# Kernel tuning notes

Measured on AMD Instinct MI355X. Metric: run time of the kernel, lower is better.

The kernel has to match this reference:

```python
import jax, jax.numpy as jnp
import numpy as np

V, E, H = 50257, 256, 256   # vocab/output_size, embed_size, hidden_size
T, B = 4096, 64             # encoder time steps, batch


def setup_inputs() -> dict:
    key = jax.random.key(0)
    ks = jax.random.split(key, 12)
    s = 0.05
    return {
        "input_ids": jax.random.randint(ks[0], (B,), 0, V),
        "hidden": jax.random.normal(ks[1], (1, B, H), dtype=jnp.float32) * s,
        "encoder_outputs": jax.random.normal(ks[2], (T, B, 2 * H), dtype=jnp.float32) * s,
        # learned parameters (PyTorch Linear convention: W @ x.T, W shape (out, in))
        "emb": jax.random.normal(ks[3], (V, E), dtype=jnp.float32) * s,
        "W_attn": jax.random.normal(ks[4], (H, 3 * H), dtype=jnp.float32) * s,
        "b_attn": jnp.zeros((H,), jnp.float32),
        "v": jax.random.normal(ks[5], (H,), dtype=jnp.float32) * s,
        "W_comb": jax.random.normal(ks[6], (H, 2 * H + E), dtype=jnp.float32) * s,
        "b_comb": jnp.zeros((H,), jnp.float32),
        "W_ih": jax.random.normal(ks[7], (3 * H, H), dtype=jnp.float32) * s,
        "W_hh": jax.random.normal(ks[8], (3 * H, H), dtype=jnp.float32) * s,
        "b_ih": jnp.zeros((3 * H,), jnp.float32),
        "b_hh": jnp.zeros((3 * H,), jnp.float32),
        "W_out": jax.random.normal(ks[9], (V, 3 * H), dtype=jnp.float32) * s,
        "b_out": jnp.zeros((V,), jnp.float32),
    }


def reference(input_ids, hidden, encoder_outputs, emb, W_attn, b_attn, v,
              W_comb, b_comb, W_ih, W_hh, b_ih, b_hh, W_out, b_out):
    Tn, Bn, _ = encoder_outputs.shape
    Hn = hidden.shape[-1]
    embedded = emb[input_ids]                 # (B, E)
    h0 = hidden[0]                            # (B, H)

    # additive (Bahdanau) attention: energies over time axis
    h_rep = jnp.broadcast_to(h0[None], (Tn, Bn, Hn))            # (T, B, H)
    cat = jnp.concatenate([h_rep, encoder_outputs], axis=2)     # (T, B, 3H)
    energies = jnp.tanh(cat @ W_attn.T + b_attn)                # (T, B, H)
    scores = jnp.einsum('tbh,h->tb', energies, v)               # (T, B)
    attn = jax.nn.softmax(scores, axis=0)                       # softmax over time
    context = jnp.einsum('tb,tbd->bd', attn, encoder_outputs)   # (B, 2H)

    # combine context with embedded input
    comb = jnp.concatenate([context, embedded], axis=1) @ W_comb.T + b_comb  # (B, H)

    # single GRU step (PyTorch gate order: r, z, n)
    gx = comb @ W_ih.T + b_ih                 # (B, 3H)
    gh = h0 @ W_hh.T + b_hh                   # (B, 3H)
    xr, xz, xn = jnp.split(gx, 3, axis=1)
    hr, hz, hn = jnp.split(gh, 3, axis=1)
    r = jax.nn.sigmoid(xr + hr)
    z = jax.nn.sigmoid(xz + hz)
    n = jnp.tanh(xn + r * hn)
    h_new = (1.0 - z) * n + z * h0            # (B, H)

    logits = jnp.concatenate([h_new, context], axis=1) @ W_out.T + b_out  # (B, V)
    logp = jax.nn.log_softmax(logits, axis=1)
    return logp, h_new[None]                  # hidden_i shape (1, B, H)
```

## Files before the change

kernel.cpp:

```cpp
#include <hip/hip_runtime.h>
#include <hip/hip_bf16.h>
#include <cstdint>
#include <cstddef>

#define Tn 4096
#define Bn 64
#define Hn 256
#define En 256
#define Vn 50257
#define D2H 512
#define K3H 768

typedef __attribute__((ext_vector_type(8))) short short8;
typedef __attribute__((ext_vector_type(4))) float f32x4;

__device__ __forceinline__ short bfs(float f)
{
    __hip_bfloat16 h = __float2bfloat16(f);
    return *reinterpret_cast<short*>(&h);
}

__device__ __forceinline__ short8 pack8(const float4 x0, const float4 x1)
{
    short8 r;
    r[0] = bfs(x0.x); r[1] = bfs(x0.y); r[2] = bfs(x0.z); r[3] = bfs(x0.w);
    r[4] = bfs(x1.x); r[5] = bfs(x1.y); r[6] = bfs(x1.z); r[7] = bfs(x1.w);
    return r;
}

__device__ __forceinline__ uint2 pack4(const float4 v)
{
    uint2 r;
    r.x = (unsigned)(unsigned short)bfs(v.x) | ((unsigned)(unsigned short)bfs(v.y) << 16);
    r.y = (unsigned)(unsigned short)bfs(v.z) | ((unsigned)(unsigned short)bfs(v.w) << 16);
    return r;
}

__device__ __forceinline__ float bf2f(unsigned short u)
{
    return __uint_as_float(((unsigned)u) << 16);
}


__global__ __launch_bounds__(256) void k1_embed_base(
    const int* __restrict__ ids, const float* __restrict__ hidden,
    const float* __restrict__ emb, const float* __restrict__ W_attn,
    const float* __restrict__ b_attn,
    float* __restrict__ baseB, float* __restrict__ emb_g)
{
    const int b = blockIdx.x, h = threadIdx.x;
    __shared__ float h0[Hn];
    h0[h] = hidden[b * Hn + h];
    __syncthreads();
    float acc = b_attn[h];
    const float* wrow = W_attn + (size_t)h * K3H;
#pragma unroll 8
    for (int k = 0; k < Hn; ++k) acc += wrow[k] * h0[k];
    baseB[b * Hn + h] = acc;
    const int id = ids[b];
    emb_g[b * En + h] = emb[(size_t)id * En + h];
}

__global__ __launch_bounds__(64) void k1b_w2frag(
    const float* __restrict__ W_attn, unsigned short* __restrict__ w2frag)
{
    const int blk = blockIdx.x;
    const int nt = blk >> 4, kb = blk & 15;
    const int l = threadIdx.x, lr = l & 15, lg = l >> 4;
    const int h = nt * 16 + lr;
    const float* src = W_attn + (size_t)h * K3H + Hn + kb * 32 + lg * 8;
    float4 x0 = *reinterpret_cast<const float4*>(src);
    float4 x1 = *reinterpret_cast<const float4*>(src + 4);
    reinterpret_cast<short8*>(w2frag)[(size_t)blk * 64 + l] = pack8(x0, x1);
}

__global__ __launch_bounds__(256, 2) void k2f_attn(
    const float* __restrict__ enc, const unsigned short* __restrict__ w2frag,
    const float* __restrict__ vvec, const float* __restrict__ baseB,
    float* __restrict__ part, float2* __restrict__ meta)
{
    const int tid = threadIdx.x;
    const int bx  = blockIdx.x;
    const int b   = bx & 63;
    const int cid = bx >> 6;
    const int l = tid & 63;
    const int w = tid >> 6;
    const int lr = l & 15, lg = l >> 4;

    __shared__ unsigned short abf[64][520];
    __shared__ float red[64][5];
    __shared__ float wts[64];

    f32x4 acc[4][4];
    const f32x4 zero = {0.f, 0.f, 0.f, 0.f};
#pragma unroll
    for (int mi = 0; mi < 4; ++mi)
#pragma unroll
        for (int ni = 0; ni < 4; ++ni) acc[mi][ni] = zero;

    const short8* wf = reinterpret_cast<const short8*>(w2frag);

    const float* gbase = enc + ((size_t)(cid * 64 + w * 16 + lg) * Bn + b) * D2H
                       + lr * 4;

#define LOADREG(dst, c) do {                                                  \
    _Pragma("unroll")                                                         \
    for (int u = 0; u < 4; ++u)                                               \
        dst[u] = *reinterpret_cast<const float4*>(                            \
            gbase + (size_t)u * 131072 + (c) * 64);                           \
    } while (0)

#define WRITEC(src, c) do {                                                   \
    _Pragma("unroll")                                                         \
    for (int u = 0; u < 4; ++u)                                               \
        *reinterpret_cast<uint2*>(&abf[w * 16 + u * 4 + lg][(c) * 64 + lr * 4])\
            = pack4(src[u]);                                                  \
    } while (0)

#define COMPUTE_KB(kb, bfr) do {                                              \
    _Pragma("unroll")                                                         \
    for (int mi = 0; mi < 4; ++mi) {                                          \
        short8 a = *reinterpret_cast<const short8*>(                          \
            &abf[mi * 16 + lr][(kb) * 32 + lg * 8]);                          \
        _Pragma("unroll")                                                     \
        for (int ni = 0; ni < 4; ++ni)                                        \
            acc[mi][ni] = __builtin_amdgcn_mfma_f32_16x16x32_bf16(            \
                a, bfr[ni], acc[mi][ni], 0, 0, 0);                            \
    } } while (0)

    float4 st0[4], st1[4];
    LOADREG(st0, 0);
    LOADREG(st1, 1);
    WRITEC(st0, 0);
    asm volatile("s_waitcnt lgkmcnt(0)" ::: "memory");
    __builtin_amdgcn_s_barrier();
    __builtin_amdgcn_sched_barrier(0);

#pragma unroll
    for (int kc = 0; kc < 8; ++kc) {
        short8 bfr0[4], bfr1[4];
#pragma unroll
        for (int ni = 0; ni < 4; ++ni)
            bfr0[ni] = wf[(size_t)(((w * 4 + ni) * 16) + 2 * kc) * 64 + l];
#pragma unroll
        for (int ni = 0; ni < 4; ++ni)
            bfr1[ni] = wf[(size_t)(((w * 4 + ni) * 16) + 2 * kc + 1) * 64 + l];
        __builtin_amdgcn_sched_barrier(0);
        if (kc < 6) {
            if ((kc & 1) == 0) LOADREG(st0, kc + 2);
            else               LOADREG(st1, kc + 2);
        }
        COMPUTE_KB(2 * kc,     bfr0);
        COMPUTE_KB(2 * kc + 1, bfr1);
        if (kc < 7) {
            if ((kc & 1) == 0) WRITEC(st1, kc + 1);
            else               WRITEC(st0, kc + 1);
        }
        asm volatile("s_waitcnt lgkmcnt(0)" ::: "memory");
        __builtin_amdgcn_s_barrier();
        __builtin_amdgcn_sched_barrier(0);
    }
#undef LOADREG
#undef WRITEC
#undef COMPUTE_KB

    float psum[4][4];
#pragma unroll
    for (int mi = 0; mi < 4; ++mi)
#pragma unroll
        for (int r = 0; r < 4; ++r) psum[mi][r] = 0.f;
#pragma unroll
    for (int ni = 0; ni < 4; ++ni) {
        const int h = w * 64 + ni * 16 + lr;
        const float vh = vvec[h];
        const float bt = baseB[b * Hn + h];
#pragma unroll
        for (int mi = 0; mi < 4; ++mi)
#pragma unroll
            for (int r = 0; r < 4; ++r)
                psum[mi][r] += vh * tanhf(acc[mi][ni][r] + bt);
    }
#pragma unroll
    for (int d = 1; d < 16; d <<= 1)
#pragma unroll
        for (int mi = 0; mi < 4; ++mi)
#pragma unroll
            for (int r = 0; r < 4; ++r)
                psum[mi][r] += __shfl_xor(psum[mi][r], d, 64);
    if (lr == 0) {
#pragma unroll
        for (int mi = 0; mi < 4; ++mi)
#pragma unroll
            for (int r = 0; r < 4; ++r)
                red[mi * 16 + lg * 4 + r][w] = psum[mi][r];
    }
    __syncthreads();

    if (tid < 64) {
        float s = red[tid][0] + red[tid][1] + red[tid][2] + red[tid][3];
        float m = s;
#pragma unroll
        for (int d = 1; d < 64; d <<= 1) m = fmaxf(m, __shfl_xor(m, d, 64));
        const float e = expf(s - m);
        float lsum = e;
#pragma unroll
        for (int d = 1; d < 64; d <<= 1) lsum += __shfl_xor(lsum, d, 64);
        wts[tid] = e;
        if (tid == 0) meta[bx] = make_float2(m, lsum);
    }
    __syncthreads();

    const int d0 = tid * 2;
    float c0 = 0.f, c1 = 0.f;
#pragma unroll 4
    for (int t = 0; t < 64; ++t) {
        const float wt = wts[t];
        const unsigned u = *reinterpret_cast<const unsigned*>(&abf[t][d0]);
        c0 += wt * bf2f((unsigned short)(u & 0xffffu));
        c1 += wt * bf2f((unsigned short)(u >> 16));
    }
    float* pp = part + (size_t)bx * 512 + d0;
    pp[0] = c0; pp[1] = c1;
}

__global__ __launch_bounds__(256) void k5n_combine(
    const float* __restrict__ part, const float2* __restrict__ meta,
    float* __restrict__ y)
{
    const int b = blockIdx.x, tid = threadIdx.x;
    __shared__ float sc[64];
    if (tid < 64) {
        const float2 ml = meta[(size_t)tid * 64 + b];
        float M = ml.x;
#pragma unroll
        for (int d = 1; d < 64; d <<= 1) M = fmaxf(M, __shfl_xor(M, d, 64));
        const float e = expf(ml.x - M);
        float L = e * ml.y;
#pragma unroll
        for (int d = 1; d < 64; d <<= 1) L += __shfl_xor(L, d, 64);
        sc[tid] = e / L;
    }
    __syncthreads();
    const int d0 = tid * 2;
    float c0 = 0.f, c1 = 0.f;
#pragma unroll 4
    for (int c = 0; c < 64; ++c) {
        const float s = sc[c];
        const float2 p = *reinterpret_cast<const float2*>(
            part + ((size_t)c * 64 + b) * 512 + d0);
        c0 += s * p.x; c1 += s * p.y;
    }
    y[(size_t)b * K3H + Hn + d0]     = c0;
    y[(size_t)b * K3H + Hn + d0 + 1] = c1;
}

__global__ __launch_bounds__(256) void k6_gru(
    const float* __restrict__ hidden, const float* __restrict__ emb_g,
    const float* __restrict__ W_comb, const float* __restrict__ b_comb,
    const float* __restrict__ W_ih, const float* __restrict__ W_hh,
    const float* __restrict__ b_ih, const float* __restrict__ b_hh,
    float* __restrict__ y, float* __restrict__ out_hidden)
{
    const int b = blockIdx.x, h = threadIdx.x;
    __shared__ float in_[K3H];
    __shared__ float h0[Hn];
    __shared__ float comb[Hn];
    __shared__ float gx[K3H], gh[K3H];
    in_[h]       = y[(size_t)b * K3H + Hn + h];
    in_[256 + h] = y[(size_t)b * K3H + Hn + 256 + h];
    in_[512 + h] = emb_g[b * En + h];
    h0[h] = hidden[b * Hn + h];
    __syncthreads();
    {
        float c = b_comb[h];
        const float* wr = W_comb + (size_t)h * K3H;
#pragma unroll 8
        for (int k = 0; k < K3H; ++k) c += wr[k] * in_[k];
        comb[h] = c;
    }
    __syncthreads();
#pragma unroll
    for (int p = 0; p < 3; ++p) {
        const int g = p * 256 + h;
        float a = b_ih[g], bh = b_hh[g];
        const float* wi = W_ih + (size_t)g * Hn;
        const float* wh = W_hh + (size_t)g * Hn;
#pragma unroll 8
        for (int k = 0; k < Hn; ++k) { a += wi[k] * comb[k]; bh += wh[k] * h0[k]; }
        gx[g] = a; gh[g] = bh;
    }
    __syncthreads();
    const float r = 1.f / (1.f + expf(-(gx[h] + gh[h])));
    const float z = 1.f / (1.f + expf(-(gx[256 + h] + gh[256 + h])));
    const float n = tanhf(gx[512 + h] + r * gh[512 + h]);
    const float hn = (1.f - z) * n + z * h0[h];
    y[(size_t)b * K3H + h] = hn;
    out_hidden[b * Hn + h] = hn;
}

__global__ __launch_bounds__(64) void k7y_pack(
    const float* __restrict__ y, unsigned short* __restrict__ yfrag)
{
    const int blk = blockIdx.x;
    const int ni = blk / 24, kb = blk % 24;
    const int l = threadIdx.x, lr = l & 15, lg = l >> 4;
    const int b = ni * 16 + lr;
    const float* src = y + (size_t)b * K3H + kb * 32 + lg * 8;
    float4 x0 = *reinterpret_cast<const float4*>(src);
    float4 x1 = *reinterpret_cast<const float4*>(src + 4);
    reinterpret_cast<short8*>(yfrag)[(size_t)blk * 64 + l] = pack8(x0, x1);
}

__global__ __launch_bounds__(256) void k7_logits(
    const float* __restrict__ W_out, const float* __restrict__ b_out,
    const unsigned short* __restrict__ yfrag, float* __restrict__ out)
{
    const int tid = threadIdx.x;
    const int vbase = blockIdx.x * 64;
    const int l = tid & 63, w = tid >> 6;
    const int lr = l & 15, lg = l >> 4;

    const short8* yf = reinterpret_cast<const short8*>(yfrag);

    f32x4 acc[4];
    const f32x4 zero = {0.f, 0.f, 0.f, 0.f};
#pragma unroll
    for (int ni = 0; ni < 4; ++ni) acc[ni] = zero;

    int v = vbase + w * 16 + lr;
    if (v >= Vn) v = Vn - 1;
    const float* wrow = W_out + (size_t)v * K3H + lg * 8;

#pragma unroll 4
    for (int kb = 0; kb < 24; ++kb) {
        float4 x0 = *reinterpret_cast<const float4*>(wrow + kb * 32);
        float4 x1 = *reinterpret_cast<const float4*>(wrow + kb * 32 + 4);
        short8 a = pack8(x0, x1);
#pragma unroll
        for (int ni = 0; ni < 4; ++ni) {
            short8 bf = yf[(size_t)(ni * 24 + kb) * 64 + l];
            acc[ni] = __builtin_amdgcn_mfma_f32_16x16x32_bf16(
                a, bf, acc[ni], 0, 0, 0);
        }
    }

    __shared__ float lt[64][65];
#pragma unroll
    for (int ni = 0; ni < 4; ++ni)
#pragma unroll
        for (int r = 0; r < 4; ++r)
            lt[w * 16 + lg * 4 + r][ni * 16 + lr] = acc[ni][r];
    __syncthreads();

#pragma unroll
    for (int u = 0; u < 16; ++u) {
        const int idx = tid + u * 256;
        const int bb = idx >> 6, vv = idx & 63;
        const int vo = vbase + vv;
        if (vo < Vn)
            out[(size_t)bb * Vn + vo] = lt[vv][bb] + b_out[vo];
    }
}

__global__ __launch_bounds__(1024) void k8_logsoftmax(float* __restrict__ out)
{
    const int b = blockIdx.x;
    float* row = out + (size_t)b * Vn;
    __shared__ float red[1024];
    float m = -1e30f;
    for (int i = threadIdx.x; i < Vn; i += 1024) m = fmaxf(m, row[i]);
    red[threadIdx.x] = m; __syncthreads();
    for (int s = 512; s > 0; s >>= 1) {
        if (threadIdx.x < s) red[threadIdx.x] = fmaxf(red[threadIdx.x], red[threadIdx.x + s]);
        __syncthreads();
    }
    m = red[0]; __syncthreads();
    float l = 0.f;
    for (int i = threadIdx.x; i < Vn; i += 1024) l += expf(row[i] - m);
    red[threadIdx.x] = l; __syncthreads();
    for (int s = 512; s > 0; s >>= 1) {
        if (threadIdx.x < s) red[threadIdx.x] += red[threadIdx.x + s];
        __syncthreads();
    }
    l = red[0];
    const float off = m + logf(l);
    for (int i = threadIdx.x; i < Vn; i += 1024) row[i] = row[i] - off;
}

extern "C" void kernel_launch(void* const* d_in, const int* in_sizes, int n_in,
                              void* d_out, int out_size, void* d_ws, size_t ws_size,
                              hipStream_t stream)
{
    const int*   ids    = (const int*)d_in[0];
    const float* hidden = (const float*)d_in[1];
    const float* enc    = (const float*)d_in[2];
    const float* emb    = (const float*)d_in[3];
    const float* W_attn = (const float*)d_in[4];
    const float* b_attn = (const float*)d_in[5];
    const float* vvec   = (const float*)d_in[6];
    const float* W_comb = (const float*)d_in[7];
    const float* b_comb = (const float*)d_in[8];
    const float* W_ih   = (const float*)d_in[9];
    const float* W_hh   = (const float*)d_in[10];
    const float* b_ih   = (const float*)d_in[11];
    const float* b_hh   = (const float*)d_in[12];
    const float* W_out  = (const float*)d_in[13];
    const float* b_out  = (const float*)d_in[14];

    float* out = (float*)d_out;
    float* ws = (float*)d_ws;
    float*  baseB = ws;
    float*  emb_g = ws + 16384;
    float2* meta  = (float2*)(ws + 32768);
    float*  part  = ws + 40960;
    float*  y     = ws + 2138112;
    unsigned short* w2frag = (unsigned short*)(ws + 2187264);
    unsigned short* yfrag  = (unsigned short*)(ws + 2252800);

    hipLaunchKernelGGL(k1_embed_base, dim3(Bn), dim3(256), 0, stream,
                       ids, hidden, emb, W_attn, b_attn, baseB, emb_g);
    hipLaunchKernelGGL(k1b_w2frag, dim3(256), dim3(64), 0, stream,
                       W_attn, w2frag);
    hipLaunchKernelGGL(k2f_attn, dim3(4096), dim3(256), 0, stream,
                       enc, w2frag, vvec, baseB, part, meta);
    hipLaunchKernelGGL(k5n_combine, dim3(Bn), dim3(256), 0, stream,
                       part, meta, y);
    hipLaunchKernelGGL(k6_gru, dim3(Bn), dim3(256), 0, stream,
                       hidden, emb_g, W_comb, b_comb, W_ih, W_hh, b_ih, b_hh,
                       y, out + (size_t)Bn * Vn);
    hipLaunchKernelGGL(k7y_pack, dim3(96), dim3(64), 0, stream, y, yfrag);
    hipLaunchKernelGGL(k7_logits, dim3((Vn + 63) / 64), dim3(256), 0, stream,
                       W_out, b_out, yfrag, out);
    hipLaunchKernelGGL(k8_logsoftmax, dim3(Bn), dim3(1024), 0, stream, out);
}
```

Before: 354.5 us.

## Triple-buffer attention loads, fuse context+GRU, split log-softmax across vocab quarters

The attention kernel now stages three register buffers instead of two, so global loads are issued one chunk further ahead of the compute. The context-combine and GRU kernels are merged into one launch, which keeps the context vector in shared memory and saves a kernel launch. Log-softmax is split into a partial-reduction kernel and an apply kernel over a 64x4 grid, using four times as many blocks for the bandwidth-bound pass over the logits. The costs are more registers in the attention kernel, which may lower occupancy, and one extra launch plus a small metadata round trip for the softmax.

Measured after the change: 341.9 us, median of 2. 3.6% less time.

```diff
diff --git a/kernel.cpp b/kernel.cpp
--- a/kernel.cpp
+++ b/kernel.cpp
@@ -128,9 +128,10 @@
                 a, bfr[ni], acc[mi][ni], 0, 0, 0);                            \
     } } while (0)
 
-    float4 st0[4], st1[4];
+    float4 st0[4], st1[4], st2[4];
     LOADREG(st0, 0);
     LOADREG(st1, 1);
+    LOADREG(st2, 2);
     WRITEC(st0, 0);
     asm volatile("s_waitcnt lgkmcnt(0)" ::: "memory");
     __builtin_amdgcn_s_barrier();
@@ -146,15 +147,18 @@
         for (int ni = 0; ni < 4; ++ni)
             bfr1[ni] = wf[(size_t)(((w * 4 + ni) * 16) + 2 * kc + 1) * 64 + l];
         __builtin_amdgcn_sched_barrier(0);
-        if (kc < 6) {
-            if ((kc & 1) == 0) LOADREG(st0, kc + 2);
-            else               LOADREG(st1, kc + 2);
+        if (kc < 5) {
+            if ((kc % 3) == 0)      LOADREG(st0, kc + 3);
+            else if ((kc % 3) == 1) LOADREG(st1, kc + 3);
+            else                    LOADREG(st2, kc + 3);
         }
         COMPUTE_KB(2 * kc,     bfr0);
         COMPUTE_KB(2 * kc + 1, bfr1);
         if (kc < 7) {
-            if ((kc & 1) == 0) WRITEC(st1, kc + 1);
-            else               WRITEC(st0, kc + 1);
+            const int wb = (kc + 1) % 3;
+            if (wb == 0)      WRITEC(st0, kc + 1);
+            else if (wb == 1) WRITEC(st1, kc + 1);
+            else              WRITEC(st2, kc + 1);
         }
         asm volatile("s_waitcnt lgkmcnt(0)" ::: "memory");
         __builtin_amdgcn_s_barrier();
@@ -223,65 +227,60 @@
     pp[0] = c0; pp[1] = c1;
 }
 
-__global__ __launch_bounds__(256) void k5n_combine(
+__global__ __launch_bounds__(256) void k56_ctx_gru(
     const float* __restrict__ part, const float2* __restrict__ meta,
-    float* __restrict__ y)
-{
-    const int b = blockIdx.x, tid = threadIdx.x;
-    __shared__ float sc[64];
-    if (tid < 64) {
-        const float2 ml = meta[(size_t)tid * 64 + b];
-        float M = ml.x;
-#pragma unroll
-        for (int d = 1; d < 64; d <<= 1) M = fmaxf(M, __shfl_xor(M, d, 64));
-        const float e = expf(ml.x - M);
-        float L = e * ml.y;
-#pragma unroll
-        for (int d = 1; d < 64; d <<= 1) L += __shfl_xor(L, d, 64);
-        sc[tid] = e / L;
-    }
-    __syncthreads();
-    const int d0 = tid * 2;
-    float c0 = 0.f, c1 = 0.f;
-#pragma unroll 4
-    for (int c = 0; c < 64; ++c) {
-        const float s = sc[c];
-        const float2 p = *reinterpret_cast<const float2*>(
-            part + ((size_t)c * 64 + b) * 512 + d0);
-        c0 += s * p.x; c1 += s * p.y;
-    }
-    y[(size_t)b * K3H + Hn + d0]     = c0;
-    y[(size_t)b * K3H + Hn + d0 + 1] = c1;
-}
-
-__global__ __launch_bounds__(256) void k6_gru(
     const float* __restrict__ hidden, const float* __restrict__ emb_g,
     const float* __restrict__ W_comb, const float* __restrict__ b_comb,
     const float* __restrict__ W_ih, const float* __restrict__ W_hh,
     const float* __restrict__ b_ih, const float* __restrict__ b_hh,
     float* __restrict__ y, float* __restrict__ out_hidden)
 {
-    const int b = blockIdx.x, h = threadIdx.x;
+    const int b = blockIdx.x, tid = threadIdx.x;
+    __shared__ float sc[64];
     __shared__ float in_[K3H];
     __shared__ float h0[Hn];
     __shared__ float comb[Hn];
     __shared__ float gx[K3H], gh[K3H];
-    in_[h]       = y[(size_t)b * K3H + Hn + h];
-    in_[256 + h] = y[(size_t)b * K3H + Hn + 256 + h];
-    in_[512 + h] = emb_g[b * En + h];
-    h0[h] = hidden[b * Hn + h];
+    if (tid < 64) {
+        const float2 ml = meta[(size_t)tid * 64 + b];
+        float M = ml.x;
+#pragma unroll
+        for (int d = 1; d < 64; d <<= 1) M = fmaxf(M, __shfl_xor(M, d, 64));
+        const float e = expf(ml.x - M);
+        float L = e * ml.y;
+#pragma unroll
+        for (int d = 1; d < 64; d <<= 1) L += __shfl_xor(L, d, 64);
+        sc[tid] = e / L;
+    }
+    in_[512 + tid] = emb_g[b * En + tid];
+    h0[tid] = hidden[b * Hn + tid];
     __syncthreads();
     {
-        float c = b_comb[h];
-        const float* wr = W_comb + (size_t)h * K3H;
+        const int d0 = tid * 2;
+        float c0 = 0.f, c1 = 0.f;
+#pragma unroll 4
+        for (int c = 0; c < 64; ++c) {
+            const float s = sc[c];
+            const float2 p = *reinterpret_cast<const float2*>(
+                part + ((size_t)c * 64 + b) * 512 + d0);
+            c0 += s * p.x; c1 += s * p.y;
+        }
+        in_[d0] = c0; in_[d0 + 1] = c1;
+        y[(size_t)b * K3H + Hn + d0]     = c0;
+        y[(size_t)b * K3H + Hn + d0 + 1] = c1;
+    }
+    __syncthreads();
+    {
+        float c = b_comb[tid];
+        const float* wr = W_comb + (size_t)tid * K3H;
 #pragma unroll 8
         for (int k = 0; k < K3H; ++k) c += wr[k] * in_[k];
-        comb[h] = c;
+        comb[tid] = c;
     }
     __syncthreads();
 #pragma unroll
     for (int p = 0; p < 3; ++p) {
-        const int g = p * 256 + h;
+        const int g = p * 256 + tid;
         float a = b_ih[g], bh = b_hh[g];
         const float* wi = W_ih + (size_t)g * Hn;
         const float* wh = W_hh + (size_t)g * Hn;
@@ -290,12 +289,12 @@
         gx[g] = a; gh[g] = bh;
     }
     __syncthreads();
-    const float r = 1.f / (1.f + expf(-(gx[h] + gh[h])));
-    const float z = 1.f / (1.f + expf(-(gx[256 + h] + gh[256 + h])));
-    const float n = tanhf(gx[512 + h] + r * gh[512 + h]);
-    const float hn = (1.f - z) * n + z * h0[h];
-    y[(size_t)b * K3H + h] = hn;
-    out_hidden[b * Hn + h] = hn;
+    const float r = 1.f / (1.f + expf(-(gx[tid] + gh[tid])));
+    const float z = 1.f / (1.f + expf(-(gx[256 + tid] + gh[256 + tid])));
+    const float n = tanhf(gx[512 + tid] + r * gh[512 + tid]);
+    const float hn = (1.f - z) * n + z * h0[tid];
+    y[(size_t)b * K3H + tid] = hn;
+    out_hidden[b * Hn + tid] = hn;
 }
 
 __global__ __launch_bounds__(64) void k7y_pack(
@@ -362,13 +361,17 @@
     }
 }
 
-__global__ __launch_bounds__(1024) void k8_logsoftmax(float* __restrict__ out)
-{
-    const int b = blockIdx.x;
-    float* row = out + (size_t)b * Vn;
+#define VQ 12565
+
+__global__ __launch_bounds__(1024) void k8a_partial(
+    const float* __restrict__ out, float2* __restrict__ qmeta)
+{
+    const int b = blockIdx.x, q = blockIdx.y;
+    const int lo = q * VQ, hi = (lo + VQ < Vn) ? lo + VQ : Vn;
+    const float* row = out + (size_t)b * Vn;
     __shared__ float red[1024];
     float m = -1e30f;
-    for (int i = threadIdx.x; i < Vn; i += 1024) m = fmaxf(m, row[i]);
+    for (int i = lo + threadIdx.x; i < hi; i += 1024) m = fmaxf(m, row[i]);
     red[threadIdx.x] = m; __syncthreads();
     for (int s = 512; s > 0; s >>= 1) {
         if (threadIdx.x < s) red[threadIdx.x] = fmaxf(red[threadIdx.x], red[threadIdx.x + s]);
@@ -376,15 +379,28 @@
     }
     m = red[0]; __syncthreads();
     float l = 0.f;
-    for (int i = threadIdx.x; i < Vn; i += 1024) l += expf(row[i] - m);
+    for (int i = lo + threadIdx.x; i < hi; i += 1024) l += expf(row[i] - m);
     red[threadIdx.x] = l; __syncthreads();
     for (int s = 512; s > 0; s >>= 1) {
         if (threadIdx.x < s) red[threadIdx.x] += red[threadIdx.x + s];
         __syncthreads();
     }
-    l = red[0];
-    const float off = m + logf(l);
-    for (int i = threadIdx.x; i < Vn; i += 1024) row[i] = row[i] - off;
+    if (threadIdx.x == 0) qmeta[b * 4 + q] = make_float2(m, red[0]);
+}
+
+__global__ __launch_bounds__(1024) void k8b_apply(
+    float* __restrict__ out, const float2* __restrict__ qmeta)
+{
+    const int b = blockIdx.x, q = blockIdx.y;
+    const int lo = q * VQ, hi = (lo + VQ < Vn) ? lo + VQ : Vn;
+    float2 q0 = qmeta[b * 4 + 0], q1 = qmeta[b * 4 + 1];
+    float2 q2 = qmeta[b * 4 + 2], q3 = qmeta[b * 4 + 3];
+    const float M = fmaxf(fmaxf(q0.x, q1.x), fmaxf(q2.x, q3.x));
+    const float L = q0.y * expf(q0.x - M) + q1.y * expf(q1.x - M)
+                  + q2.y * expf(q2.x - M) + q3.y * expf(q3.x - M);
+    const float off = M + logf(L);
+    float* row = out + (size_t)b * Vn;
+    for (int i = lo + threadIdx.x; i < hi; i += 1024) row[i] -= off;
 }
 
 extern "C" void kernel_launch(void* const* d_in, const int* in_sizes, int n_in,
@@ -416,6 +432,7 @@
     float*  y     = ws + 2138112;
     unsigned short* w2frag = (unsigned short*)(ws + 2187264);
     unsigned short* yfrag  = (unsigned short*)(ws + 2252800);
+    float2* qmeta = (float2*)(ws + 2277376);
 
     hipLaunchKernelGGL(k1_embed_base, dim3(Bn), dim3(256), 0, stream,
                        ids, hidden, emb, W_attn, b_attn, baseB, emb_g);
@@ -423,13 +440,14 @@
                        W_attn, w2frag);
     hipLaunchKernelGGL(k2f_attn, dim3(4096), dim3(256), 0, stream,
                        enc, w2frag, vvec, baseB, part, meta);
-    hipLaunchKernelGGL(k5n_combine, dim3(Bn), dim3(256), 0, stream,
-                       part, meta, y);
-    hipLaunchKernelGGL(k6_gru, dim3(Bn), dim3(256), 0, stream,
-                       hidden, emb_g, W_comb, b_comb, W_ih, W_hh, b_ih, b_hh,
-                       y, out + (size_t)Bn * Vn);
+    hipLaunchKernelGGL(k56_ctx_gru, dim3(Bn), dim3(256), 0, stream,
+                       part, meta, hidden, emb_g, W_comb, b_comb,
+                       W_ih, W_hh, b_ih, b_hh, y, out + (size_t)Bn * Vn);
     hipLaunchKernelGGL(k7y_pack, dim3(96), dim3(64), 0, stream, y, yfrag);
     hipLaunchKernelGGL(k7_logits, dim3((Vn + 63) / 64), dim3(256), 0, stream,
                        W_out, b_out, yfrag, out);
-    hipLaunchKernelGGL(k8_logsoftmax, dim3(Bn), dim3(1024), 0, stream, out);
-}
+    hipLaunchKernelGGL(k8a_partial, dim3(Bn, 4), dim3(1024), 0, stream,
+                       out, qmeta);
+    hipLaunchKernelGGL(k8b_apply, dim3(Bn, 4), dim3(1024), 0, stream,
+                       out, qmeta);
+}
```
